# Optimization experiments

Measured on AMD Instinct MI355X. Metric: run time of the kernel, lower is better.

The kernel has to match this reference:

```python
import jax, jax.numpy as jnp
import numpy as np

B, T, D, H = 4, 2048, 512, 8
DH = D // H  # 64
EPS = 1e-5


def setup_inputs() -> dict:
    key = jax.random.key(0)
    ks = jax.random.split(key, 12)
    s = lambda k, shp, fan: jax.random.normal(k, shp, jnp.float32) * (fan ** -0.5)
    return {
        "x": jax.random.normal(ks[0], (B, T, D), jnp.float32),
        "ln1_g": jnp.ones((D,), jnp.float32),
        "ln1_b": jnp.zeros((D,), jnp.float32),
        "Wq": s(ks[1], (H, D, DH), D),  # per-head bias-free projections
        "Wk": s(ks[2], (H, D, DH), D),
        "Wv": s(ks[3], (H, D, DH), D),
        "Wproj": s(ks[4], (D, D), D),
        "bproj": jnp.zeros((D,), jnp.float32),
        "W1": s(ks[5], (D, 4 * D), D),
        "b1": jnp.zeros((4 * D,), jnp.float32),
        "W2": s(ks[6], (4 * D, D), 4 * D),
        "b2": jnp.zeros((D,), jnp.float32),
    }


def _layernorm(x, g, b):
    m = jnp.mean(x, axis=-1, keepdims=True)
    v = jnp.var(x, axis=-1, keepdims=True)
    return (x - m) * jax.lax.rsqrt(v + EPS) * g + b


def reference(x, ln1_g, ln1_b, Wq, Wk, Wv, Wproj, bproj, W1, b1, W2, b2):
    b, t, c = x.shape
    scale = c ** -0.5  # source scales by input channel dim, not head_size
    causal = jnp.tril(jnp.ones((t, t), bool))  # [T,T]

    # --- attention sublayer (pre-norm with ln1) ---
    h = _layernorm(x, ln1_g, ln1_b)
    q = jnp.einsum('btd,hde->bhte', h, Wq)
    k = jnp.einsum('btd,hde->bhte', h, Wk)
    v = jnp.einsum('btd,hde->bhte', h, Wv)
    scores = jnp.einsum('bhte,bhse->bhts', q, k) * scale  # [B,H,T,T]
    scores = jnp.where(causal, scores, -jnp.inf)
    att = jax.nn.softmax(scores, axis=-1)  # dropout = identity at inference
    o = jnp.einsum('bhts,bhse->bthe', att, v).reshape(b, t, c)  # concat heads
    sa = o @ Wproj + bproj
    x = x + sa

    # --- FFN sublayer (source reuses ln1, faithful) ---
    h2 = _layernorm(x, ln1_g, ln1_b)
    ff = jax.nn.relu(h2 @ W1 + b1) @ W2 + b2
    return x + ff
```

## Files before the change

### kernel.cpp

```cpp
#include <hip/hip_runtime.h>
#include <math.h>

#define B_ 4
#define T_ 2048
#define D_ 512
#define H_ 8
#define DH_ 64
#define BT_ 8192
#define FF_ 2048
#define EPS_ 1e-5f
#define SCALE_ 0.04419417382415922f
#define SC2_ 0.06375861151f
#define NEGINF_ -1e30f

typedef short b16x8 __attribute__((ext_vector_type(8)));
typedef short b16x4 __attribute__((ext_vector_type(4)));
typedef float f32x4 __attribute__((ext_vector_type(4)));

#define MFMA16(a, b, c) __builtin_amdgcn_mfma_f32_16x16x32_bf16(a, b, c, 0, 0, 0)
#define MFMA16K16(a, b, c) __builtin_amdgcn_mfma_f32_16x16x16bf16_1k(a, b, c, 0, 0, 0)

#define GLL16(gp, lp) \
    __builtin_amdgcn_global_load_lds((const __attribute__((address_space(1))) void*)(gp), \
                                     (__attribute__((address_space(3))) void*)(lp), 16, 0, 0)

#if __has_builtin(__builtin_amdgcn_exp2f)
#define EXP2F(x) __builtin_amdgcn_exp2f(x)
#else
#define EXP2F(x) exp2f(x)
#endif

static __device__ inline short f2bf(float f) {
    unsigned int u = __builtin_bit_cast(unsigned int, f);
    unsigned int r = (u + 0x7fffu + ((u >> 16) & 1u)) >> 16;
    return (short)r;
}
static __device__ inline short f2bf_trunc(float f) {
    return (short)(__builtin_bit_cast(unsigned int, f) >> 16);
}
static __device__ inline float bf2f(short s) {
    return __builtin_bit_cast(float, ((unsigned int)(unsigned short)s) << 16);
}

__global__ __launch_bounds__(256) void ln_kernel(const float* __restrict__ X,
        const float* __restrict__ G, const float* __restrict__ Bb,
        short* __restrict__ Y)
{
    int wave = threadIdx.x >> 6, t = threadIdx.x & 63;
    int row = blockIdx.x * 4 + wave;
    const float* xr = X + (size_t)row * D_;
    float4 v0 = *(const float4*)(xr + t * 4);
    float4 v1 = *(const float4*)(xr + 256 + t * 4);
    float sum = v0.x + v0.y + v0.z + v0.w + v1.x + v1.y + v1.z + v1.w;
    float ssq = v0.x*v0.x + v0.y*v0.y + v0.z*v0.z + v0.w*v0.w
              + v1.x*v1.x + v1.y*v1.y + v1.z*v1.z + v1.w*v1.w;
    #pragma unroll
    for (int off = 32; off > 0; off >>= 1) {
        sum += __shfl_down(sum, off);
        ssq += __shfl_down(ssq, off);
    }
    sum = __shfl(sum, 0);
    ssq = __shfl(ssq, 0);
    float mean = sum * (1.0f / D_);
    float var  = ssq * (1.0f / D_) - mean * mean;
    float rstd = rsqrtf(var + EPS_);

    float4 g0 = *(const float4*)(G + t * 4);
    float4 g1 = *(const float4*)(G + 256 + t * 4);
    float4 b0 = *(const float4*)(Bb + t * 4);
    float4 b1 = *(const float4*)(Bb + 256 + t * 4);
    short4 o0, o1;
    o0.x = f2bf((v0.x - mean) * rstd * g0.x + b0.x);
    o0.y = f2bf((v0.y - mean) * rstd * g0.y + b0.y);
    o0.z = f2bf((v0.z - mean) * rstd * g0.z + b0.z);
    o0.w = f2bf((v0.w - mean) * rstd * g0.w + b0.w);
    o1.x = f2bf((v1.x - mean) * rstd * g1.x + b1.x);
    o1.y = f2bf((v1.y - mean) * rstd * g1.y + b1.y);
    o1.z = f2bf((v1.z - mean) * rstd * g1.z + b1.z);
    o1.w = f2bf((v1.w - mean) * rstd * g1.w + b1.w);
    short* yr = Y + (size_t)row * D_;
    *(short4*)(yr + t * 4)       = o0;
    *(short4*)(yr + 256 + t * 4) = o1;
}

__global__ __launch_bounds__(256) void prep_kernel(
        const float* __restrict__ Wq, const float* __restrict__ Wk,
        const float* __restrict__ Wv, const float* __restrict__ Wp,
        const float* __restrict__ W1, const float* __restrict__ W2,
        short* __restrict__ wqkv, short* __restrict__ wpt,
        short* __restrict__ w1t, short* __restrict__ w2t)
{
    __shared__ float tile[32][33];
    int idx = blockIdx.x;
    const float* src; short* dst; int R, C, tx0, ty0;
    if (idx < 768) {
        int w = idx >> 8, rem = idx & 255;
        int hh = rem >> 5, t = rem & 31;
        const float* base = (w == 0) ? Wq : ((w == 1) ? Wk : Wv);
        src = base + hh * (D_ * DH_);
        dst = wqkv + w * (512 * 512) + hh * (DH_ * D_);
        R = 512; C = 64; tx0 = (t & 1) * 32; ty0 = (t >> 1) * 32;
    } else if (idx < 1024) {
        int t = idx - 768;
        src = Wp; dst = wpt; R = 512; C = 512;
        tx0 = (t & 15) * 32; ty0 = (t >> 4) * 32;
    } else if (idx < 2048) {
        int t = idx - 1024;
        src = W1; dst = w1t; R = 512; C = 2048;
        tx0 = (t & 63) * 32; ty0 = (t >> 6) * 32;
    } else {
        int t = idx - 2048;
        src = W2; dst = w2t; R = 2048; C = 512;
        tx0 = (t & 15) * 32; ty0 = (t >> 4) * 32;
    }
    int tx = threadIdx.x, ty = threadIdx.y;
    #pragma unroll
    for (int i = 0; i < 32; i += 8)
        tile[ty + i][tx] = src[(size_t)(ty0 + ty + i) * C + tx0 + tx];
    __syncthreads();
    #pragma unroll
    for (int i = 0; i < 32; i += 8)
        dst[(size_t)(tx0 + ty + i) * R + ty0 + tx] = f2bf(tile[tx][ty + i]);
}

__global__ __launch_bounds__(256) void mm64_kernel(const short* __restrict__ A,
        const short* __restrict__ Bt, void* __restrict__ C,
        const float* __restrict__ bias, const float* __restrict__ resid,
        int M, int N, int K, int relu, int out_bf16)
{
    __shared__ short As[2][128 * 32];
    __shared__ short Bs[2][64 * 32];
    const int tid = threadIdx.x;
    const int wave = tid >> 6, lane = tid & 63;
    const int quad = lane >> 4, l15 = lane & 15;
    const int m0 = blockIdx.x * 128, n0 = blockIdx.y * 64;
    const int mw = (wave & 1) * 64, nw = (wave >> 1) * 32;

#define STAGE_M64(bufi, kk) \
    { \
        for (int r = 0; r < 2; ++r) { \
            int c = r * 256 + tid; \
            int row = c >> 2, seg = (c & 3) ^ ((row >> 1) & 3); \
            GLL16(A + (size_t)(m0 + row) * K + (kk) + seg * 8, \
                  As[bufi] + (size_t)(r * 256 + wave * 64) * 8); \
        } \
        { \
            int row = tid >> 2, seg = (tid & 3) ^ ((row >> 1) & 3); \
            GLL16(Bt + (size_t)(n0 + row) * K + (kk) + seg * 8, \
                  Bs[bufi] + (size_t)(wave * 64) * 8); \
        } \
    }

    f32x4 acc[4][2];
    #pragma unroll
    for (int i = 0; i < 4; ++i)
        #pragma unroll
        for (int j = 0; j < 2; ++j)
            acc[i][j] = (f32x4){0.f, 0.f, 0.f, 0.f};

    STAGE_M64(0, 0);
    int buf = 0;
    for (int k0 = 0; k0 < K; k0 += 32) {
        __syncthreads();
        if (k0 + 32 < K) STAGE_M64(buf ^ 1, k0 + 32);
        b16x8 af[4], bf[2];
        #pragma unroll
        for (int i = 0; i < 4; ++i) {
            int row = mw + i * 16 + l15;
            af[i] = *(const b16x8*)(As[buf] + row * 32 + ((quad ^ ((row >> 1) & 3)) * 8));
        }
        #pragma unroll
        for (int j = 0; j < 2; ++j) {
            int row = nw + j * 16 + l15;
            bf[j] = *(const b16x8*)(Bs[buf] + row * 32 + ((quad ^ ((row >> 1) & 3)) * 8));
        }
        #pragma unroll
        for (int i = 0; i < 4; ++i)
            #pragma unroll
            for (int j = 0; j < 2; ++j)
                acc[i][j] = MFMA16(af[i], bf[j], acc[i][j]);
        buf ^= 1;
    }
#undef STAGE_M64

    #pragma unroll
    for (int i = 0; i < 4; ++i) {
        #pragma unroll
        for (int r = 0; r < 4; ++r) {
            size_t row = (size_t)(m0 + mw + i * 16 + quad * 4 + r);
            #pragma unroll
            for (int j = 0; j < 2; ++j) {
                int col = n0 + nw + j * 16 + l15;
                float v = acc[i][j][r];
                if (bias)  v += bias[col];
                if (resid) v += resid[row * N + col];
                if (relu)  v = fmaxf(v, 0.0f);
                if (out_bf16) ((short*)C)[row * N + col] = f2bf(v);
                else          ((float*)C)[row * N + col] = v;
            }
        }
    }
}

__global__ __launch_bounds__(256) void mm6464_kernel(const short* __restrict__ A,
        const short* __restrict__ Bt, void* __restrict__ C,
        const float* __restrict__ bias, const float* __restrict__ resid,
        int M, int N, int K, int relu, int out_bf16)
{
    __shared__ short As[2][64 * 64];
    __shared__ short Bs[2][64 * 64];
    const int tid = threadIdx.x;
    const int wave = tid >> 6, lane = tid & 63;
    const int quad = lane >> 4, l15 = lane & 15;
    const int m0 = blockIdx.x * 64, n0 = blockIdx.y * 64;
    const int nw = wave * 16;

#define STAGE_M66(bufi, kk) \
    { \
        for (int r = 0; r < 2; ++r) { \
            int c = r * 256 + tid; \
            int row = c >> 3, seg = (c & 7) ^ (row & 7); \
            GLL16(A + (size_t)(m0 + row) * K + (kk) + seg * 8, \
                  As[bufi] + (size_t)(r * 256 + wave * 64) * 8); \
            GLL16(Bt + (size_t)(n0 + row) * K + (kk) + seg * 8, \
                  Bs[bufi] + (size_t)(r * 256 + wave * 64) * 8); \
        } \
    }

    f32x4 acc[4];
    #pragma unroll
    for (int i = 0; i < 4; ++i) acc[i] = (f32x4){0.f, 0.f, 0.f, 0.f};

    STAGE_M66(0, 0);
    int buf = 0;
    for (int k0 = 0; k0 < K; k0 += 64) {
        __syncthreads();
        if (k0 + 64 < K) STAGE_M66(buf ^ 1, k0 + 64);
        b16x8 af[4][2], bf[2];
        #pragma unroll
        for (int i = 0; i < 4; ++i)
            #pragma unroll
            for (int kb = 0; kb < 2; ++kb) {
                int row = i * 16 + l15;
                af[i][kb] = *(const b16x8*)(As[buf] + row * 64 + (((kb * 4 + quad) ^ (row & 7)) * 8));
            }
        #pragma unroll
        for (int kb = 0; kb < 2; ++kb) {
            int row = nw + l15;
            bf[kb] = *(const b16x8*)(Bs[buf] + row * 64 + (((kb * 4 + quad) ^ (row & 7)) * 8));
        }
        #pragma unroll
        for (int kb = 0; kb < 2; ++kb)
            #pragma unroll
            for (int i = 0; i < 4; ++i)
                acc[i] = MFMA16(af[i][kb], bf[kb], acc[i]);
        buf ^= 1;
    }
#undef STAGE_M66

    #pragma unroll
    for (int i = 0; i < 4; ++i) {
        #pragma unroll
        for (int r = 0; r < 4; ++r) {
            size_t row = (size_t)(m0 + i * 16 + quad * 4 + r);
            int col = n0 + nw + l15;
            float v = acc[i][r];
            if (bias)  v += bias[col];
            if (resid) v += resid[row * N + col];
            if (relu)  v = fmaxf(v, 0.0f);
            if (out_bf16) ((short*)C)[row * N + col] = f2bf(v);
            else          ((float*)C)[row * N + col] = v;
        }
    }
}

__global__ __launch_bounds__(256) void attn_kernel(const short* __restrict__ qkv,
        short* __restrict__ Opart, float* __restrict__ Ml)
{
    __shared__ short Qs[64 * 72];
    __shared__ short Ks[64 * 64];
    __shared__ short Vt[64 * 64];

    const int tid = threadIdx.x;
    const int wave = tid >> 6, lane = tid & 63;
    const int quad = lane >> 4, l15 = lane & 15;
    const int bh = blockIdx.x;
    const int qi = 31 - (int)blockIdx.y;
    const int split = blockIdx.z;
    const int b = bh >> 3, h = bh & 7;
    const size_t tok0 = (size_t)b * T_;
    const int qrow_rel = wave * 16 + l15;
    const int half = (qi + 1) >> 1;
    const int klo = split ? half : 0;
    const int khi = split ? qi + 1 : half;
    const int pidx = split * 1024 + bh * 32 + qi;
    short* Op = Opart + (size_t)pidx * 4096;
    float* mlp = Ml + (size_t)pidx * 64;

    if (klo >= khi) {
        for (int i = tid; i < 2048; i += 256) ((int*)Op)[i] = 0;
        if (tid < 64) mlp[tid] = 0.0f;
        return;
    }

    #pragma unroll
    for (int r = 0; r < 2; ++r) {
        int c = r * 256 + tid;
        int tk = c >> 3;
        int seg = (c & 7) ^ (tk & 7);
        GLL16(qkv + (tok0 + qi * 64 + tk) * 1536 + h * 64 + seg * 8,
              Qs + (size_t)(r * 256 + wave * 64) * 8);
    }

    float lrow = 0.0f;
    f32x4 ot[4];
    #pragma unroll
    for (int dt = 0; dt < 4; ++dt) ot[dt] = (f32x4){0.f, 0.f, 0.f, 0.f};

    b16x8 qf[2];

    for (int kj = klo; kj < khi; ++kj) {
        __syncthreads();
        #pragma unroll
        for (int r = 0; r < 2; ++r) {
            int c = r * 256 + tid;
            int tk = c >> 3;
            int seg = (c & 7) ^ (tk & 7);
            GLL16(qkv + (tok0 + kj * 64 + tk) * 1536 + 512 + h * 64 + seg * 8,
                  Ks + (size_t)(r * 256 + wave * 64) * 8);
        }
        {
            int s = tid >> 5, tp = tid & 31;
            const short* g0 = qkv + (tok0 + kj * 64 + tp * 2) * 1536 + 1024 + h * 64 + s * 8;
            b16x8 v0 = *(const b16x8*)g0;
            b16x8 v1 = *(const b16x8*)(g0 + 1536);
            int* vo = (int*)Vt;
            int gg = tp >> 1, hlf = tp & 1;
            #pragma unroll
            for (int e = 0; e < 8; ++e) {
                int row = s * 8 + e;
                unsigned int pk = (unsigned int)(unsigned short)v0[e]
                                | ((unsigned int)(unsigned short)v1[e] << 16);
                vo[row * 32 + ((gg ^ (row & 15)) << 1) + hlf] = pk;
            }
        }
        __syncthreads();

        if (kj == klo) {
            #pragma unroll
            for (int kb = 0; kb < 2; ++kb) {
                int row = wave * 16 + l15;
                qf[kb] = *(const b16x8*)(Qs + row * 64 + (((kb * 4 + quad) ^ (row & 7)) * 8));
            }
        }

        f32x4 st[4];
        #pragma unroll
        for (int mt = 0; mt < 4; ++mt) st[mt] = (f32x4){0.f, 0.f, 0.f, 0.f};
        #pragma unroll
        for (int mt = 0; mt < 4; ++mt) {
            int trow = mt * 16 + l15;
            #pragma unroll
            for (int kb = 0; kb < 2; ++kb) {
                b16x8 kf = *(const b16x8*)(Ks + trow * 64 + (((kb * 4 + quad) ^ (trow & 7)) * 8));
                st[mt] = MFMA16(kf, qf[kb], st[mt]);
            }
        }

        const bool diag = (kj == qi);
        float rs = 0.0f;
        b16x4 pf[4];
        #pragma unroll
        for (int mt = 0; mt < 4; ++mt)
            #pragma unroll
            for (int r = 0; r < 4; ++r) {
                float s = st[mt][r];
                if (diag && (mt * 16 + quad * 4 + r) > qrow_rel) s = NEGINF_;
                float e = EXP2F(s * SC2_);
                rs += e;
                pf[mt][r] = f2bf_trunc(e);
            }
        rs += __shfl_xor(rs, 16);
        rs += __shfl_xor(rs, 32);
        lrow += rs;
        #pragma unroll
        for (int dt = 0; dt < 4; ++dt) {
            const short* vrow = Vt + (dt * 16 + l15) * 64;
            #pragma unroll
            for (int kt = 0; kt < 4; ++kt) {
                b16x4 vf = *(const b16x4*)(vrow + (((kt * 4 + quad) ^ l15) << 2));
                ot[dt] = MFMA16K16(vf, pf[kt], ot[dt]);
            }
        }
    }

    __syncthreads();
    float inv = 1.0f / lrow;
    #pragma unroll
    for (int dt = 0; dt < 4; ++dt) {
        b16x4 o4;
        o4[0] = f2bf(ot[dt][0] * inv);
        o4[1] = f2bf(ot[dt][1] * inv);
        o4[2] = f2bf(ot[dt][2] * inv);
        o4[3] = f2bf(ot[dt][3] * inv);
        *(b16x4*)(Qs + (size_t)qrow_rel * 72 + dt * 16 + quad * 4) = o4;
    }
    {
        int row = tid >> 2, ch = tid & 3;
        b16x8 lo = *(const b16x8*)(Qs + (size_t)row * 72 + ch * 16);
        b16x8 hi = *(const b16x8*)(Qs + (size_t)row * 72 + ch * 16 + 8);
        short* dst = Op + row * 64 + ch * 16;
        *(b16x8*)dst = lo;
        *(b16x8*)(dst + 8) = hi;
    }
    if (quad == 0) mlp[qrow_rel] = lrow;
}

__global__ __launch_bounds__(256) void attn_combine_kernel(
        const short* __restrict__ Opart, const float* __restrict__ Ml,
        short* __restrict__ Ob)
{
    int pair = blockIdx.x;
    int bh = pair >> 5, qi = pair & 31;
    int b = bh >> 3, h = bh & 7;
    int tid = threadIdx.x;
    const short* O1 = Opart + (size_t)pair * 4096;
    const short* O2 = Opart + (size_t)(1024 + pair) * 4096;
    const float* ml1 = Ml + (size_t)pair * 64;
    const float* ml2 = Ml + (size_t)(1024 + pair) * 64;
    int ch = tid & 7;
    #pragma unroll
    for (int it = 0; it < 2; ++it) {
        int row = it * 32 + (tid >> 3);
        float l1 = ml1[row], l2 = ml2[row];
        float inv = 1.0f / (l1 + l2);
        float w1 = l1 * inv, w2 = l2 * inv;
        b16x8 a = *(const b16x8*)(O1 + row * 64 + ch * 8);
        b16x8 c = *(const b16x8*)(O2 + row * 64 + ch * 8);
        b16x8 o;
        #pragma unroll
        for (int e = 0; e < 8; ++e)
            o[e] = f2bf(w1 * bf2f(a[e]) + w2 * bf2f(c[e]));
        short* dst = Ob + ((size_t)(b * T_ + qi * 64 + row)) * 512 + h * 64 + ch * 8;
        *(b16x8*)dst = o;
    }
}

extern "C" void kernel_launch(void* const* d_in, const int* in_sizes, int n_in,
                              void* d_out, int out_size, void* d_ws, size_t ws_size,
                              hipStream_t stream) {
    (void)in_sizes; (void)n_in; (void)out_size; (void)ws_size;
    const float* x     = (const float*)d_in[0];
    const float* ln_g  = (const float*)d_in[1];
    const float* ln_b  = (const float*)d_in[2];
    const float* Wq    = (const float*)d_in[3];
    const float* Wk    = (const float*)d_in[4];
    const float* Wv    = (const float*)d_in[5];
    const float* Wproj = (const float*)d_in[6];
    const float* bproj = (const float*)d_in[7];
    const float* W1    = (const float*)d_in[8];
    const float* b1    = (const float*)d_in[9];
    const float* W2    = (const float*)d_in[10];
    const float* b2    = (const float*)d_in[11];
    float* out = (float*)d_out;

    char* W = (char*)d_ws;
    short* hbuf  = (short*)(W + 0);
    short* qkvb  = (short*)(W + ((size_t)8  << 20));
    short* attno = (short*)(W + ((size_t)32 << 20));
    float* x1    = (float*)(W + ((size_t)40 << 20));
    short* ff1   = (short*)(W + ((size_t)56 << 20));
    short* wqkv  = (short*)(W + ((size_t)88 << 20));
    short* wpt   = (short*)(W + ((size_t)90 << 20));
    short* w1t   = (short*)(W + ((size_t)91 << 20));
    short* w2t   = (short*)(W + ((size_t)93 << 20));
    short* Opart = (short*)(W + ((size_t)96 << 20));
    float* Ml    = (float*)(W + ((size_t)112 << 20));

    prep_kernel<<<dim3(3072), dim3(32, 8), 0, stream>>>(
        Wq, Wk, Wv, Wproj, W1, W2, wqkv, wpt, w1t, w2t);
    ln_kernel<<<dim3(BT_ / 4), dim3(256), 0, stream>>>(x, ln_g, ln_b, hbuf);
    mm64_kernel<<<dim3(64, 24), dim3(256), 0, stream>>>(hbuf, wqkv, qkvb,
        nullptr, nullptr, BT_, 1536, D_, 0, 1);
    attn_kernel<<<dim3(32, 32, 2), dim3(256), 0, stream>>>(qkvb, Opart, Ml);
    attn_combine_kernel<<<dim3(1024), dim3(256), 0, stream>>>(Opart, Ml, attno);
    mm6464_kernel<<<dim3(128, 8), dim3(256), 0, stream>>>(attno, wpt, x1,
        bproj, x, BT_, D_, D_, 0, 0);
    ln_kernel<<<dim3(BT_ / 4), dim3(256), 0, stream>>>(x1, ln_g, ln_b, hbuf);
    mm64_kernel<<<dim3(64, 32), dim3(256), 0, stream>>>(hbuf, w1t, ff1,
        b1, nullptr, BT_, FF_, D_, 1, 1);
    mm6464_kernel<<<dim3(128, 8), dim3(256), 0, stream>>>(ff1, w2t, out,
        b2, x1, BT_, D_, FF_, 0, 0);
}
```

Before: 257.1 us.

## Replace both GEMM kernels with a single-wave 64x64-tile MFMA kernel

Merges the two GEMM variants into one kernel where a single 64-lane wave computes a full 64x64 output tile with a 4x4 grid of MFMA accumulators. Because the block is a single wave, it drops __syncthreads and issues the next stage's global-to-LDS loads after reading the current buffer into registers. The aim is more register-level reuse per wave and no block barriers. In exchange, each block has a quarter of the threads, latency hiding per CU may drop, and the long-K projection GEMMs now run as one wave per tile. Correctness depends on the async LDS loads completing before they are read without an explicit barrier.

```diff
diff --git a/kernel.cpp b/kernel.cpp
--- a/kernel.cpp
+++ b/kernel.cpp
@@ -123,74 +123,68 @@
         dst[(size_t)(tx0 + ty + i) * R + ty0 + tx] = f2bf(tile[tx][ty + i]);
 }
 
-__global__ __launch_bounds__(256) void mm64_kernel(const short* __restrict__ A,
+__global__ __launch_bounds__(64) void mmw_kernel(const short* __restrict__ A,
         const short* __restrict__ Bt, void* __restrict__ C,
         const float* __restrict__ bias, const float* __restrict__ resid,
         int M, int N, int K, int relu, int out_bf16)
 {
-    __shared__ short As[2][128 * 32];
+    __shared__ short As[2][64 * 32];
     __shared__ short Bs[2][64 * 32];
-    const int tid = threadIdx.x;
-    const int wave = tid >> 6, lane = tid & 63;
+    const int lane = threadIdx.x;
     const int quad = lane >> 4, l15 = lane & 15;
-    const int m0 = blockIdx.x * 128, n0 = blockIdx.y * 64;
-    const int mw = (wave & 1) * 64, nw = (wave >> 1) * 32;
-
-#define STAGE_M64(bufi, kk) \
+    const int m0 = blockIdx.x * 64, n0 = blockIdx.y * 64;
+    const int srow = lane >> 2;
+    const int schunk = lane & 3;
+
+#define STAGEW(bufi, kk) \
     { \
-        for (int r = 0; r < 2; ++r) { \
-            int c = r * 256 + tid; \
-            int row = c >> 2, seg = (c & 3) ^ ((row >> 1) & 3); \
+        _Pragma("unroll") \
+        for (int r = 0; r < 4; ++r) { \
+            int row = r * 16 + srow; \
+            int seg = schunk ^ ((row >> 1) & 3); \
             GLL16(A + (size_t)(m0 + row) * K + (kk) + seg * 8, \
-                  As[bufi] + (size_t)(r * 256 + wave * 64) * 8); \
+                  As[bufi] + r * 512); \
+            GLL16(Bt + (size_t)(n0 + row) * K + (kk) + seg * 8, \
+                  Bs[bufi] + r * 512); \
         } \
-        { \
-            int row = tid >> 2, seg = (tid & 3) ^ ((row >> 1) & 3); \
-            GLL16(Bt + (size_t)(n0 + row) * K + (kk) + seg * 8, \
-                  Bs[bufi] + (size_t)(wave * 64) * 8); \
-        } \
-    }
-
-    f32x4 acc[4][2];
+    }
+
+    f32x4 acc[4][4];
     #pragma unroll
     for (int i = 0; i < 4; ++i)
         #pragma unroll
-        for (int j = 0; j < 2; ++j)
+        for (int j = 0; j < 4; ++j)
             acc[i][j] = (f32x4){0.f, 0.f, 0.f, 0.f};
 
-    STAGE_M64(0, 0);
+    STAGEW(0, 0);
     int buf = 0;
     for (int k0 = 0; k0 < K; k0 += 32) {
-        __syncthreads();
-        if (k0 + 32 < K) STAGE_M64(buf ^ 1, k0 + 32);
-        b16x8 af[4], bf[2];
+        b16x8 af[4], bf[4];
         #pragma unroll
         for (int i = 0; i < 4; ++i) {
-            int row = mw + i * 16 + l15;
-            af[i] = *(const b16x8*)(As[buf] + row * 32 + ((quad ^ ((row >> 1) & 3)) * 8));
-        }
-        #pragma unroll
-        for (int j = 0; j < 2; ++j) {
-            int row = nw + j * 16 + l15;
-            bf[j] = *(const b16x8*)(Bs[buf] + row * 32 + ((quad ^ ((row >> 1) & 3)) * 8));
-        }
+            int row = i * 16 + l15;
+            int c = quad ^ ((row >> 1) & 3);
+            af[i] = *(const b16x8*)(As[buf] + row * 32 + c * 8);
+            bf[i] = *(const b16x8*)(Bs[buf] + row * 32 + c * 8);
+        }
+        if (k0 + 32 < K) STAGEW(buf ^ 1, k0 + 32);
         #pragma unroll
         for (int i = 0; i < 4; ++i)
             #pragma unroll
-            for (int j = 0; j < 2; ++j)
+            for (int j = 0; j < 4; ++j)
                 acc[i][j] = MFMA16(af[i], bf[j], acc[i][j]);
         buf ^= 1;
     }
-#undef STAGE_M64
+#undef STAGEW
 
     #pragma unroll
     for (int i = 0; i < 4; ++i) {
         #pragma unroll
         for (int r = 0; r < 4; ++r) {
-            size_t row = (size_t)(m0 + mw + i * 16 + quad * 4 + r);
-            #pragma unroll
-            for (int j = 0; j < 2; ++j) {
-                int col = n0 + nw + j * 16 + l15;
+            size_t row = (size_t)(m0 + i * 16 + quad * 4 + r);
+            #pragma unroll
+            for (int j = 0; j < 4; ++j) {
+                int col = n0 + j * 16 + l15;
                 float v = acc[i][j][r];
                 if (bias)  v += bias[col];
                 if (resid) v += resid[row * N + col];
@@ -198,78 +192,6 @@
                 if (out_bf16) ((short*)C)[row * N + col] = f2bf(v);
                 else          ((float*)C)[row * N + col] = v;
             }
-        }
-    }
-}
-
-__global__ __launch_bounds__(256) void mm6464_kernel(const short* __restrict__ A,
-        const short* __restrict__ Bt, void* __restrict__ C,
-        const float* __restrict__ bias, const float* __restrict__ resid,
-        int M, int N, int K, int relu, int out_bf16)
-{
-    __shared__ short As[2][64 * 64];
-    __shared__ short Bs[2][64 * 64];
-    const int tid = threadIdx.x;
-    const int wave = tid >> 6, lane = tid & 63;
-    const int quad = lane >> 4, l15 = lane & 15;
-    const int m0 = blockIdx.x * 64, n0 = blockIdx.y * 64;
-    const int nw = wave * 16;
-
-#define STAGE_M66(bufi, kk) \
-    { \
-        for (int r = 0; r < 2; ++r) { \
-            int c = r * 256 + tid; \
-            int row = c >> 3, seg = (c & 7) ^ (row & 7); \
-            GLL16(A + (size_t)(m0 + row) * K + (kk) + seg * 8, \
-                  As[bufi] + (size_t)(r * 256 + wave * 64) * 8); \
-            GLL16(Bt + (size_t)(n0 + row) * K + (kk) + seg * 8, \
-                  Bs[bufi] + (size_t)(r * 256 + wave * 64) * 8); \
-        } \
-    }
-
-    f32x4 acc[4];
-    #pragma unroll
-    for (int i = 0; i < 4; ++i) acc[i] = (f32x4){0.f, 0.f, 0.f, 0.f};
-
-    STAGE_M66(0, 0);
-    int buf = 0;
-    for (int k0 = 0; k0 < K; k0 += 64) {
-        __syncthreads();
-        if (k0 + 64 < K) STAGE_M66(buf ^ 1, k0 + 64);
-        b16x8 af[4][2], bf[2];
-        #pragma unroll
-        for (int i = 0; i < 4; ++i)
-            #pragma unroll
-            for (int kb = 0; kb < 2; ++kb) {
-                int row = i * 16 + l15;
-                af[i][kb] = *(const b16x8*)(As[buf] + row * 64 + (((kb * 4 + quad) ^ (row & 7)) * 8));
-            }
-        #pragma unroll
-        for (int kb = 0; kb < 2; ++kb) {
-            int row = nw + l15;
-            bf[kb] = *(const b16x8*)(Bs[buf] + row * 64 + (((kb * 4 + quad) ^ (row & 7)) * 8));
-        }
-        #pragma unroll
-        for (int kb = 0; kb < 2; ++kb)
-            #pragma unroll
-            for (int i = 0; i < 4; ++i)
-                acc[i] = MFMA16(af[i][kb], bf[kb], acc[i]);
-        buf ^= 1;
-    }
-#undef STAGE_M66
-
-    #pragma unroll
-    for (int i = 0; i < 4; ++i) {
-        #pragma unroll
-        for (int r = 0; r < 4; ++r) {
-            size_t row = (size_t)(m0 + i * 16 + quad * 4 + r);
-            int col = n0 + nw + l15;
-            float v = acc[i][r];
-            if (bias)  v += bias[col];
-            if (resid) v += resid[row * N + col];
-            if (relu)  v = fmaxf(v, 0.0f);
-            if (out_bf16) ((short*)C)[row * N + col] = f2bf(v);
-            else          ((float*)C)[row * N + col] = v;
         }
     }
 }
@@ -480,15 +402,15 @@
     prep_kernel<<<dim3(3072), dim3(32, 8), 0, stream>>>(
         Wq, Wk, Wv, Wproj, W1, W2, wqkv, wpt, w1t, w2t);
     ln_kernel<<<dim3(BT_ / 4), dim3(256), 0, stream>>>(x, ln_g, ln_b, hbuf);
-    mm64_kernel<<<dim3(64, 24), dim3(256), 0, stream>>>(hbuf, wqkv, qkvb,
+    mmw_kernel<<<dim3(128, 24), dim3(64), 0, stream>>>(hbuf, wqkv, qkvb,
         nullptr, nullptr, BT_, 1536, D_, 0, 1);
     attn_kernel<<<dim3(32, 32, 2), dim3(256), 0, stream>>>(qkvb, Opart, Ml);
     attn_combine_kernel<<<dim3(1024), dim3(256), 0, stream>>>(Opart, Ml, attno);
-    mm6464_kernel<<<dim3(128, 8), dim3(256), 0, stream>>>(attno, wpt, x1,
+    mmw_kernel<<<dim3(128, 8), dim3(64), 0, stream>>>(attno, wpt, x1,
         bproj, x, BT_, D_, D_, 0, 0);
     ln_kernel<<<dim3(BT_ / 4), dim3(256), 0, stream>>>(x1, ln_g, ln_b, hbuf);
-    mm64_kernel<<<dim3(64, 32), dim3(256), 0, stream>>>(hbuf, w1t, ff1,
+    mmw_kernel<<<dim3(128, 32), dim3(64), 0, stream>>>(hbuf, w1t, ff1,
         b1, nullptr, BT_, FF_, D_, 1, 1);
-    mm6464_kernel<<<dim3(128, 8), dim3(256), 0, stream>>>(ff1, w2t, out,
+    mmw_kernel<<<dim3(128, 8), dim3(64), 0, stream>>>(ff1, w2t, out,
         b2, x1, BT_, D_, FF_, 0, 0);
 }
```

Result: slower. 320.7 us (+24.7%).
